# Kernel optimization log

Measured on AMD Instinct MI355X. Metric: run time of the kernel, lower is better.

The kernel has to match this reference:

```python
import jax, jax.numpy as jnp
import numpy as np

NUM_POINTS = 17  # number of t quadrature points
T_MAX = 2.0
VAR_GAMMA = 1.0
B, D, K = 8192, 2048, 512


def setup_inputs() -> dict:
    key = jax.random.key(0)
    k1, k2 = jax.random.split(key)
    embeddings = jax.random.normal(k1, (B, D), dtype=jnp.float32)
    directions = jax.random.normal(k2, (D, K), dtype=jnp.float32)
    return {"embeddings": embeddings, "directions": directions}


def reference(embeddings, directions):
    z = embeddings.astype(jnp.float32)

    # VICReg-style variance floor on raw embedding dims (unbiased std, as torch)
    cls_std = jnp.std(z, axis=0, ddof=1)
    var_floor = jnp.mean(jax.nn.relu(VAR_GAMMA - cls_std))

    # F.normalize(directions, dim=0): divide by column L2 norm (clamped at 1e-12)
    norms = jnp.maximum(jnp.linalg.norm(directions, axis=0, keepdims=True), 1e-12)
    d = directions / norms

    proj = z @ d  # (B, K)
    std = jnp.std(proj, axis=0, ddof=1)
    proj = (proj - jnp.mean(proj, axis=0, keepdims=True)) / (std + 1e-8)

    # Trapezoid quadrature over t in (0, T_MAX]
    t = jnp.linspace(0.0, T_MAX, NUM_POINTS + 1)[1:]          # (T,)
    dt = T_MAX / NUM_POINTS
    w = jnp.full((NUM_POINTS,), dt).at[0].set(dt / 2).at[-1].set(dt / 2)

    # All t-points in one fused pass: (T, B, K)
    tp = t[:, None, None] * proj[None, :, :]
    ecf_real = jnp.mean(jnp.cos(tp), axis=1)                  # (T, K)
    ecf_imag = jnp.mean(jnp.sin(tp), axis=1)                  # (T, K)
    tcf = jnp.exp(-0.5 * t * t)[:, None]                      # (T, 1) target CF N(0,1)

    integrand = ecf_real ** 2 + ecf_imag ** 2 - 2.0 * ecf_real * tcf + tcf ** 2
    total = jnp.sum(w * jnp.mean(integrand, axis=1))
    return total + var_floor
```

## Files before the change

kernel.cpp:

```cpp
#include <hip/hip_runtime.h>
#include <hip/hip_bf16.h>

#define BB   8192
#define DD   2048
#define KK   512
#define TT   17

#define BM   128
#define BN   128
#define BK   128
#define NT   (DD / BK)

#define NZB  512
#define NDB  16

typedef __attribute__((ext_vector_type(8))) short  bf16x8;
typedef __attribute__((ext_vector_type(4))) float  f32x4;

__device__ __forceinline__ void gload16(const void* g, void* l) {
  __builtin_amdgcn_global_load_lds(
      (const __attribute__((address_space(1))) void*)g,
      (__attribute__((address_space(3))) void*)l,
      16, 0, 0);
}

__global__ __launch_bounds__(256) void prep_z_kernel(
    const float* __restrict__ z, unsigned short* __restrict__ zb,
    float* __restrict__ part2) {
  int c = threadIdx.x * 8;
  int r0 = blockIdx.x * 16;
  float s[8] = {0,0,0,0,0,0,0,0}, ss[8] = {0,0,0,0,0,0,0,0};
  for (int ch = 0; ch < 4; ++ch) {
    float4 u[4][2];
    #pragma unroll
    for (int rr = 0; rr < 4; ++rr) {
      const float* p = &z[(size_t)(r0 + ch * 4 + rr) * DD + c];
      u[rr][0] = *(const float4*)p;
      u[rr][1] = *(const float4*)(p + 4);
    }
    #pragma unroll
    for (int rr = 0; rr < 4; ++rr) {
      float f[8] = {u[rr][0].x, u[rr][0].y, u[rr][0].z, u[rr][0].w,
                    u[rr][1].x, u[rr][1].y, u[rr][1].z, u[rr][1].w};
      bf16x8 o;
      #pragma unroll
      for (int i = 0; i < 8; ++i) {
        s[i] += f[i]; ss[i] += f[i] * f[i];
        __hip_bfloat16 h = __float2bfloat16(f[i]);
        o[i] = *(short*)&h;
      }
      *(bf16x8*)&zb[(size_t)(r0 + ch * 4 + rr) * DD + c] = o;
    }
  }
  float* pb = part2 + (size_t)blockIdx.x * 4096;
  *(float4*)&pb[c]        = (float4){s[0], s[1], s[2], s[3]};
  *(float4*)&pb[c + 4]    = (float4){s[4], s[5], s[6], s[7]};
  *(float4*)&pb[2048 + c]     = (float4){ss[0], ss[1], ss[2], ss[3]};
  *(float4*)&pb[2048 + c + 4] = (float4){ss[4], ss[5], ss[6], ss[7]};
}

__global__ __launch_bounds__(256) void reduce2_kernel(
    const float* __restrict__ part2, float* __restrict__ colsum,
    float* __restrict__ colsumsq, const float* __restrict__ dir,
    float* __restrict__ part3) {
  int bid = blockIdx.x;
  int tid = threadIdx.x;
  if (bid < 32) {
    int d = bid * 64 + (tid & 63);
    int ch = tid >> 6;
    float s = 0.f, q = 0.f;
    for (int b = ch * 128; b < ch * 128 + 128; ++b) {
      s += part2[(size_t)b * 4096 + d];
      q += part2[(size_t)b * 4096 + 2048 + d];
    }
    __shared__ float rs[4][64], rq[4][64];
    rs[ch][tid & 63] = s; rq[ch][tid & 63] = q;
    __syncthreads();
    if (tid < 64) {
      colsum[d]   = rs[0][tid] + rs[1][tid] + rs[2][tid] + rs[3][tid];
      colsumsq[d] = rq[0][tid] + rq[1][tid] + rq[2][tid] + rq[3][tid];
    }
  } else {
    int b2 = bid - 32;
    int kxi = b2 & 1, ry = b2 >> 1;
    int k = kxi * 256 + tid;
    int r0 = ry * (DD / NDB);
    float ss = 0.f;
    for (int r = r0; r < r0 + DD / NDB; ++r) {
      float v = dir[(size_t)r * KK + k];
      ss += v * v;
    }
    part3[(size_t)ry * KK + k] = ss;
  }
}

__global__ __launch_bounds__(256) void finalize1_kernel(
    const float* __restrict__ colsum, const float* __restrict__ colsumsq,
    const float* __restrict__ part3, float* __restrict__ invnorm,
    float* __restrict__ out, float* __restrict__ psum) {
  int tid = threadIdx.x;
  for (int i = tid; i < 2 * KK; i += 256) psum[i] = 0.f;
  for (int k = tid; k < KK; k += 256) {
    float ssq = 0.f;
    #pragma unroll
    for (int i = 0; i < NDB; ++i) ssq += part3[(size_t)i * KK + k];
    float n = sqrtf(ssq);
    invnorm[k] = 1.0f / fmaxf(n, 1e-12f);
  }
  float acc = 0.f;
  for (int d = tid; d < DD; d += 256) {
    float s = colsum[d], ss = colsumsq[d];
    float var = (ss - s * s / (float)BB) / (float)(BB - 1);
    float sd = sqrtf(fmaxf(var, 0.f));
    acc += fmaxf(1.0f - sd, 0.0f);
  }
  __shared__ float red[256];
  red[tid] = acc; __syncthreads();
  for (int s = 128; s > 0; s >>= 1) {
    if (tid < s) red[tid] += red[tid + s];
    __syncthreads();
  }
  if (tid == 0) out[0] = red[0] / (float)DD;
}

__global__ __launch_bounds__(256) void dirT_kernel(
    const float* __restrict__ dir, const float* __restrict__ invnorm,
    unsigned short* __restrict__ dT) {
  __shared__ unsigned short tile[64][65];
  int n0 = blockIdx.x * 64;
  int d0 = blockIdx.y * 64;
  int tx = threadIdx.x & 63, ty = threadIdx.x >> 6;
  float inv = invnorm[n0 + tx];
  #pragma unroll
  for (int i = 0; i < 16; ++i) {
    int dr = ty + i * 4;
    float v = dir[(size_t)(d0 + dr) * KK + n0 + tx] * inv;
    __hip_bfloat16 h = __float2bfloat16(v);
    tile[dr][tx] = *(unsigned short*)&h;
  }
  __syncthreads();
  #pragma unroll
  for (int i = 0; i < 16; ++i) {
    int nr = ty + i * 4;
    dT[(size_t)(n0 + nr) * DD + d0 + tx] = tile[tx][nr];
  }
}

__global__ __launch_bounds__(256) void gemm_bf16_kernel(
    const unsigned short* __restrict__ zb, const unsigned short* __restrict__ dT,
    float* __restrict__ proj, float* __restrict__ psum, float* __restrict__ psumsq) {
  __shared__ __align__(16) short As[2][BM * BK];
  __shared__ __align__(16) short Bs[2][BN * BK];

  int tid = threadIdx.x;
  int w = tid >> 6, l = tid & 63;

  int bid = blockIdx.x;
  int xcd = bid & 7, slot = bid >> 3;
  int bmi = xcd * 8 + (slot >> 2);
  int bni = slot & 3;
  int bm = bmi * BM, bn = bni * BN;

  int r4 = l >> 4;
  int gsw_e = ((l & 15) ^ r4) * 8;
  int gsw_o = ((l & 15) ^ (r4 + 4)) * 8;
  const unsigned short* aRow = zb + (size_t)(bm + w * 32 + r4) * DD;
  const unsigned short* bRow = dT + (size_t)(bn + w * 32 + r4) * DD;

#define STAGE(buf, kt) do {                                                   \
    const unsigned short* a_ = aRow + (size_t)(kt) * BK;                      \
    const unsigned short* b_ = bRow + (size_t)(kt) * BK;                      \
    gload16(a_ + 0 * 4 * DD + gsw_e, &As[buf][(w * 32 + 0) * BK]);            \
    gload16(b_ + 0 * 4 * DD + gsw_e, &Bs[buf][(w * 32 + 0) * BK]);            \
    gload16(a_ + 1 * 4 * DD + gsw_o, &As[buf][(w * 32 + 4) * BK]);            \
    gload16(b_ + 1 * 4 * DD + gsw_o, &Bs[buf][(w * 32 + 4) * BK]);            \
    gload16(a_ + 2 * 4 * DD + gsw_e, &As[buf][(w * 32 + 8) * BK]);            \
    gload16(b_ + 2 * 4 * DD + gsw_e, &Bs[buf][(w * 32 + 8) * BK]);            \
    gload16(a_ + 3 * 4 * DD + gsw_o, &As[buf][(w * 32 + 12) * BK]);           \
    gload16(b_ + 3 * 4 * DD + gsw_o, &Bs[buf][(w * 32 + 12) * BK]);           \
    gload16(a_ + 4 * 4 * DD + gsw_e, &As[buf][(w * 32 + 16) * BK]);           \
    gload16(b_ + 4 * 4 * DD + gsw_e, &Bs[buf][(w * 32 + 16) * BK]);           \
    gload16(a_ + 5 * 4 * DD + gsw_o, &As[buf][(w * 32 + 20) * BK]);           \
    gload16(b_ + 5 * 4 * DD + gsw_o, &Bs[buf][(w * 32 + 20) * BK]);           \
    gload16(a_ + 6 * 4 * DD + gsw_e, &As[buf][(w * 32 + 24) * BK]);           \
    gload16(b_ + 6 * 4 * DD + gsw_e, &Bs[buf][(w * 32 + 24) * BK]);           \
    gload16(a_ + 7 * 4 * DD + gsw_o, &As[buf][(w * 32 + 28) * BK]);           \
    gload16(b_ + 7 * 4 * DD + gsw_o, &Bs[buf][(w * 32 + 28) * BK]);           \
  } while (0)

  int wm = (w >> 1) * 64, wn = (w & 1) * 64;
  int fr = l & 15, fq = l >> 4;
  int fx = fr & 7;

  f32x4 acc[4][4];
  f32x4 zero4 = {0.f, 0.f, 0.f, 0.f};
  #pragma unroll
  for (int mi = 0; mi < 4; ++mi)
    #pragma unroll
    for (int ni = 0; ni < 4; ++ni) acc[mi][ni] = zero4;

  STAGE(0, 0);
  asm volatile("s_waitcnt vmcnt(0)" ::: "memory");
  __builtin_amdgcn_s_barrier();

  for (int t = 0; t < NT; ++t) {
    int cur = t & 1;
    if (t + 1 < NT) STAGE(cur ^ 1, t + 1);
    #pragma unroll
    for (int kk = 0; kk < 4; ++kk) {
      bf16x8 av[4], bv[4];
      int go = ((kk * 4 + fq) ^ fx) * 8;
      #pragma unroll
      for (int mi = 0; mi < 4; ++mi)
        av[mi] = *(const bf16x8*)&As[cur][(wm + mi * 16 + fr) * BK + go];
      #pragma unroll
      for (int ni = 0; ni < 4; ++ni)
        bv[ni] = *(const bf16x8*)&Bs[cur][(wn + ni * 16 + fr) * BK + go];
      #pragma unroll
      for (int mi = 0; mi < 4; ++mi)
        #pragma unroll
        for (int ni = 0; ni < 4; ++ni)
          acc[mi][ni] = __builtin_amdgcn_mfma_f32_16x16x32_bf16(av[mi], bv[ni], acc[mi][ni], 0, 0, 0);
    }
    asm volatile("s_waitcnt vmcnt(0)" ::: "memory");
    __builtin_amdgcn_s_barrier();
  }
#undef STAGE

  #pragma unroll
  for (int ni = 0; ni < 4; ++ni) {
    float s = 0.f, q = 0.f;
    int col = bn + wn + ni * 16 + fr;
    #pragma unroll
    for (int mi = 0; mi < 4; ++mi)
      #pragma unroll
      for (int j = 0; j < 4; ++j) {
        float v = acc[mi][ni][j];
        s += v; q += v * v;
        proj[(size_t)(bm + wm + mi * 16 + fq * 4 + j) * KK + col] = v;
      }
    s += __shfl_xor(s, 16); q += __shfl_xor(q, 16);
    s += __shfl_xor(s, 32); q += __shfl_xor(q, 32);
    if (fq == 0) {
      atomicAdd(&psum[col], s);
      atomicAdd(&psumsq[col], q);
    }
  }
}

__global__ __launch_bounds__(256) void ecf_kernel(
    const float* __restrict__ proj, const float* __restrict__ psum,
    const float* __restrict__ psumsq, float* __restrict__ part) {
  int kx = blockIdx.x, ry = blockIdx.y;
  int tid = threadIdx.x;
  int kl = tid & 63, w = tid >> 6;
  int k = kx * 64 + kl;
  float sk = psum[k], qk = psumsq[k];
  float m = sk / (float)BB;
  float var = (qk - sk * sk / (float)BB) / (float)(BB - 1);
  float sd = sqrtf(fmaxf(var, 0.f));
  float is = 1.0f / (sd + 1e-8f);
  int r0 = ry * 128 + w * 32;
  const float dt = 2.0f / 17.0f;

  float ac[TT], as[TT];
  #pragma unroll
  for (int j = 0; j < TT; ++j) { ac[j] = 0.f; as[j] = 0.f; }

  #pragma unroll 4
  for (int i = 0; i < 32; ++i) {
    float p = (proj[(size_t)(r0 + i) * KK + k] - m) * is;
    float th = dt * p;
    float s1, c1;
    __sincosf(th, &s1, &c1);
    float tc = 2.0f * c1;
    float cj = c1, sj = s1, cjm = 1.0f, sjm = 0.0f;
    ac[0] += c1; as[0] += s1;
    #pragma unroll
    for (int j = 1; j < TT; ++j) {
      float cn = tc * cj - cjm;
      float sn = tc * sj - sjm;
      cjm = cj; sjm = sj; cj = cn; sj = sn;
      ac[j] += cj; as[j] += sj;
    }
  }

  __shared__ float red[4 * 2176];
  int base = w * 2176 + kl * 34;
  #pragma unroll
  for (int j = 0; j < TT; ++j) {
    red[base + j] = ac[j];
    red[base + 17 + j] = as[j];
  }
  __syncthreads();
  for (int idx = tid; idx < 2176; idx += 256) {
    float v = red[idx] + red[2176 + idx] + red[4352 + idx] + red[6528 + idx];
    part[(size_t)(ry * 8 + kx) * 2176 + idx] = v;
  }
}

__global__ __launch_bounds__(256) void ecf_final_kernel(
    const float* __restrict__ part, float* __restrict__ out) {
  int gi = blockIdx.x * 256 + threadIdx.x;
  int kx = gi / 1088;
  int r2 = gi - kx * 1088;
  int kl = r2 / 17;
  int j  = r2 - kl * 17;
  const float dt = 2.0f / 17.0f;
  float cs = 0.f, ss = 0.f;
  for (int ry = 0; ry < 64; ++ry) {
    size_t b = (size_t)(ry * 8 + kx) * 2176 + kl * 34;
    cs += part[b + j];
    ss += part[b + 17 + j];
  }
  const float invB = 1.0f / (float)BB;
  float r  = cs * invB;
  float im = ss * invB;
  float t = dt * (float)(j + 1);
  float wq = (j == 0 || j == TT - 1) ? dt * 0.5f : dt;
  float tcf = expf(-0.5f * t * t);
  float val = wq * (r * r + im * im - 2.0f * r * tcf + tcf * tcf) / (float)KK;

  __shared__ float red[256];
  int tid = threadIdx.x;
  red[tid] = val; __syncthreads();
  for (int s = 128; s > 0; s >>= 1) {
    if (tid < s) red[tid] += red[tid + s];
    __syncthreads();
  }
  if (tid == 0) atomicAdd(out, red[0]);
}

extern "C" void kernel_launch(void* const* d_in, const int* in_sizes, int n_in,
                              void* d_out, int out_size, void* d_ws, size_t ws_size,
                              hipStream_t stream) {
  const float* z   = (const float*)d_in[0];
  const float* dir = (const float*)d_in[1];
  float* out = (float*)d_out;

  uint8_t* w8 = (uint8_t*)d_ws;
  unsigned short* zb = (unsigned short*)w8;
  float* part        = (float*)w8;
  unsigned short* dT = (unsigned short*)(w8 + 33554432);
  float* proj        = (float*)(w8 + 35651584);
  float* part2       = (float*)(w8 + 35651584);
  float* stat        = (float*)(w8 + 52428800);
  float* colsum   = stat;
  float* colsumsq = colsum + DD;
  float* psum     = colsumsq + DD;
  float* psumsq   = psum + KK;
  float* invnorm  = psumsq + KK;
  float* part3    = invnorm + KK;

  prep_z_kernel<<<dim3(NZB), 256, 0, stream>>>(z, zb, part2);
  reduce2_kernel<<<dim3(64), 256, 0, stream>>>(part2, colsum, colsumsq, dir, part3);
  finalize1_kernel<<<1, 256, 0, stream>>>(colsum, colsumsq, part3, invnorm, out, psum);
  dirT_kernel<<<dim3(8, 32), 256, 0, stream>>>(dir, invnorm, dT);
  gemm_bf16_kernel<<<dim3(256), 256, 0, stream>>>(zb, dT, proj, psum, psumsq);
  ecf_kernel<<<dim3(8, 64), 256, 0, stream>>>(proj, psum, psumsq, part);
  ecf_final_kernel<<<dim3(34), 256, 0, stream>>>(part, out);
}
```

Measured before the change: 115.7 us.

## Split column-statistics and direction-norm reductions across more blocks with vector loads

The reduction kernel that sums per-block column statistics now launches 256 blocks instead of 32. Each block covers a quarter of the batch partials, and the sum and sum-of-squares halves are handled by separate blocks, so more of the GPU is used on this memory-bound pass. The direction-column-norm part now uses float4 loads, 32 row groups and an in-block shared-memory combine. This adds an extra partial-sum level that finalize1 folds in. The cost is a little more workspace traffic and a slightly longer serial loop in the single-block finalize kernel.

New measurement: 102.3 us. -11.6%, faster.

```diff
diff --git a/kernel.cpp b/kernel.cpp
--- a/kernel.cpp
+++ b/kernel.cpp
@@ -12,7 +12,6 @@
 #define NT   (DD / BK)
 
 #define NZB  512
-#define NDB  16
 
 typedef __attribute__((ext_vector_type(8))) short  bf16x8;
 typedef __attribute__((ext_vector_type(4))) float  f32x4;
@@ -60,56 +59,68 @@
 }
 
 __global__ __launch_bounds__(256) void reduce2_kernel(
-    const float* __restrict__ part2, float* __restrict__ colsum,
-    float* __restrict__ colsumsq, const float* __restrict__ dir,
-    float* __restrict__ part3) {
+    const float* __restrict__ part2, float* __restrict__ part5,
+    const float* __restrict__ dir, float* __restrict__ part3) {
   int bid = blockIdx.x;
   int tid = threadIdx.x;
-  if (bid < 32) {
-    int d = bid * 64 + (tid & 63);
+  if (bid < 256) {
+    int dgrp = bid & 63, bq = bid >> 6;
+    int d = dgrp * 64 + (tid & 63);
     int ch = tid >> 6;
-    float s = 0.f, q = 0.f;
-    for (int b = ch * 128; b < ch * 128 + 128; ++b) {
+    int b0 = bq * 128 + ch * 32;
+    float s = 0.f;
+    for (int b = b0; b < b0 + 32; ++b)
       s += part2[(size_t)b * 4096 + d];
-      q += part2[(size_t)b * 4096 + 2048 + d];
-    }
-    __shared__ float rs[4][64], rq[4][64];
-    rs[ch][tid & 63] = s; rq[ch][tid & 63] = q;
+    __shared__ float rs[4][64];
+    rs[ch][tid & 63] = s;
     __syncthreads();
-    if (tid < 64) {
-      colsum[d]   = rs[0][tid] + rs[1][tid] + rs[2][tid] + rs[3][tid];
-      colsumsq[d] = rq[0][tid] + rq[1][tid] + rq[2][tid] + rq[3][tid];
-    }
+    if (tid < 64)
+      part5[(size_t)bq * 4096 + dgrp * 64 + tid] =
+          rs[0][tid] + rs[1][tid] + rs[2][tid] + rs[3][tid];
   } else {
-    int b2 = bid - 32;
-    int kxi = b2 & 1, ry = b2 >> 1;
-    int k = kxi * 256 + tid;
-    int r0 = ry * (DD / NDB);
-    float ss = 0.f;
-    for (int r = r0; r < r0 + DD / NDB; ++r) {
-      float v = dir[(size_t)r * KK + k];
-      ss += v * v;
-    }
-    part3[(size_t)ry * KK + k] = ss;
+    int rg = bid - 256;
+    int c4 = tid & 127;
+    int half = tid >> 7;
+    int r0 = rg * 64 + half;
+    float4 q = {0.f, 0.f, 0.f, 0.f};
+    #pragma unroll 8
+    for (int i = 0; i < 32; ++i) {
+      float4 v = *(const float4*)&dir[(size_t)(r0 + 2 * i) * KK + c4 * 4];
+      q.x += v.x * v.x; q.y += v.y * v.y; q.z += v.z * v.z; q.w += v.w * v.w;
+    }
+    __shared__ float rd[2][512];
+    *(float4*)&rd[half][c4 * 4] = q;
+    __syncthreads();
+    if (tid < 128) {
+      float4 a = *(float4*)&rd[0][tid * 4];
+      float4 b = *(float4*)&rd[1][tid * 4];
+      float4 o = {a.x + b.x, a.y + b.y, a.z + b.z, a.w + b.w};
+      *(float4*)&part3[(size_t)rg * KK + tid * 4] = o;
+    }
   }
 }
 
 __global__ __launch_bounds__(256) void finalize1_kernel(
-    const float* __restrict__ colsum, const float* __restrict__ colsumsq,
-    const float* __restrict__ part3, float* __restrict__ invnorm,
-    float* __restrict__ out, float* __restrict__ psum) {
+    const float* __restrict__ part5, const float* __restrict__ part3,
+    float* __restrict__ invnorm, float* __restrict__ out,
+    float* __restrict__ psum) {
   int tid = threadIdx.x;
   for (int i = tid; i < 2 * KK; i += 256) psum[i] = 0.f;
   for (int k = tid; k < KK; k += 256) {
     float ssq = 0.f;
     #pragma unroll
-    for (int i = 0; i < NDB; ++i) ssq += part3[(size_t)i * KK + k];
+    for (int i = 0; i < 32; ++i) ssq += part3[(size_t)i * KK + k];
     float n = sqrtf(ssq);
     invnorm[k] = 1.0f / fmaxf(n, 1e-12f);
   }
   float acc = 0.f;
   for (int d = tid; d < DD; d += 256) {
-    float s = colsum[d], ss = colsumsq[d];
+    float s = 0.f, ss = 0.f;
+    #pragma unroll
+    for (int i = 0; i < 4; ++i) {
+      s  += part5[i * 4096 + d];
+      ss += part5[i * 4096 + 2048 + d];
+    }
     float var = (ss - s * s / (float)BB) / (float)(BB - 1);
     float sd = sqrtf(fmaxf(var, 0.f));
     acc += fmaxf(1.0f - sd, 0.0f);
@@ -345,16 +356,15 @@
   float* proj        = (float*)(w8 + 35651584);
   float* part2       = (float*)(w8 + 35651584);
   float* stat        = (float*)(w8 + 52428800);
-  float* colsum   = stat;
-  float* colsumsq = colsum + DD;
-  float* psum     = colsumsq + DD;
+  float* part5    = stat;
+  float* psum     = part5 + 16384;
   float* psumsq   = psum + KK;
   float* invnorm  = psumsq + KK;
   float* part3    = invnorm + KK;
 
   prep_z_kernel<<<dim3(NZB), 256, 0, stream>>>(z, zb, part2);
-  reduce2_kernel<<<dim3(64), 256, 0, stream>>>(part2, colsum, colsumsq, dir, part3);
-  finalize1_kernel<<<1, 256, 0, stream>>>(colsum, colsumsq, part3, invnorm, out, psum);
+  reduce2_kernel<<<dim3(288), 256, 0, stream>>>(part2, part5, dir, part3);
+  finalize1_kernel<<<1, 256, 0, stream>>>(part5, part3, invnorm, out, psum);
   dirT_kernel<<<dim3(8, 32), 256, 0, stream>>>(dir, invnorm, dT);
   gemm_bf16_kernel<<<dim3(256), 256, 0, stream>>>(zb, dT, proj, psum, psumsq);
   ecf_kernel<<<dim3(8, 64), 256, 0, stream>>>(proj, psum, psumsq, part);
```
